# Kernel tuning notes

Hardware: AMD Instinct MI355X
Metric: run time of the kernel (lower is better)

Reference implementation:

```python
import jax, jax.numpy as jnp
import numpy as np
import math

B, T, D, H = 2, 2048, 1024, 16
HD = D // H  # head_dim = 64
DFF = 4 * D
EPS = 1e-5


def gelu_tanh(x):
    c = math.sqrt(2.0 / math.pi)
    return 0.5 * x * (1.0 + jnp.tanh(c * (x + 0.044715 * x ** 3)))


def layernorm(x, scale, shift):
    mean = jnp.mean(x, axis=-1, keepdims=True)
    var = jnp.mean((x - mean) ** 2, axis=-1, keepdims=True)
    return scale * (x - mean) / jnp.sqrt(var + EPS) + shift


def setup_inputs() -> dict:
    key = jax.random.key(0)
    ks = jax.random.split(key, 10)
    s_in = 1.0 / math.sqrt(D)
    s_ff = 1.0 / math.sqrt(DFF)
    return {
        "x": jax.random.normal(ks[0], (B, T, D), dtype=jnp.float32),
        "Wq": jax.random.normal(ks[1], (D, D), dtype=jnp.float32) * s_in,
        "Wk": jax.random.normal(ks[2], (D, D), dtype=jnp.float32) * s_in,
        "Wv": jax.random.normal(ks[3], (D, D), dtype=jnp.float32) * s_in,
        "Wo": jax.random.normal(ks[4], (D, D), dtype=jnp.float32) * s_in,
        "bo": jnp.zeros((D,), dtype=jnp.float32),
        "W1": jax.random.normal(ks[5], (D, DFF), dtype=jnp.float32) * s_in,
        "b1": jnp.zeros((DFF,), dtype=jnp.float32),
        "W2": jax.random.normal(ks[6], (DFF, D), dtype=jnp.float32) * s_ff,
        "b2": jnp.zeros((D,), dtype=jnp.float32),
        "g1": jnp.ones((D,), dtype=jnp.float32),
        "s1": jnp.zeros((D,), dtype=jnp.float32),
        "g2": jnp.ones((D,), dtype=jnp.float32),
        "s2": jnp.zeros((D,), dtype=jnp.float32),
    }


def reference(x, Wq, Wk, Wv, Wo, bo, W1, b1, W2, b2, g1, s1, g2, s2):
    # --- attention sublayer (pre-LN) ---
    h = layernorm(x, g1, s1)
    q = (h @ Wq).reshape(B, T, H, HD).transpose(0, 2, 1, 3)  # [B,H,T,hd]
    k = (h @ Wk).reshape(B, T, H, HD).transpose(0, 2, 1, 3)
    v = (h @ Wv).reshape(B, T, H, HD).transpose(0, 2, 1, 3)
    scores = jnp.einsum('bhqd,bhkd->bhqk', q, k) / math.sqrt(HD)
    causal = jnp.triu(jnp.ones((T, T), dtype=bool), k=1)
    scores = jnp.where(causal, -jnp.inf, scores)
    attn = jax.nn.softmax(scores, axis=-1)
    ctx = jnp.einsum('bhqk,bhkd->bhqd', attn, v)
    ctx = ctx.transpose(0, 2, 1, 3).reshape(B, T, D)
    x = x + (ctx @ Wo + bo)
    # --- feed-forward sublayer (pre-LN) ---
    h2 = layernorm(x, g2, s2)
    ff = gelu_tanh(h2 @ W1 + b1) @ W2 + b2
    return x + ff
```

## Files before the change

### kernel.cpp

```cpp
#include <hip/hip_runtime.h>
#include <cstdint>
#include <cstddef>

typedef unsigned short u16;
typedef __attribute__((ext_vector_type(8))) __bf16 bf16x8;
typedef __attribute__((ext_vector_type(8))) unsigned short u16x8;
typedef __attribute__((ext_vector_type(4))) float f32x4;
typedef __attribute__((ext_vector_type(16))) float f32x16;
typedef __attribute__((ext_vector_type(4))) unsigned short u16x4;
typedef __attribute__((ext_vector_type(2))) int i32x2;

#define DEV __device__ __forceinline__

DEV u16 f2bf(float f) {
  union { float f; unsigned u; } v; v.f = f;
  unsigned r = v.u + 0x7fffu + ((v.u >> 16) & 1u);
  return (u16)(r >> 16);
}

DEV float bf2f(u16 b) {
  unsigned u = ((unsigned)b) << 16;
  union { unsigned u; float f; } v; v.u = u;
  return v.f;
}

DEV void gload_lds16(const void* g, void* l) {
  __builtin_amdgcn_global_load_lds(
      (const __attribute__((address_space(1))) void*)g,
      (__attribute__((address_space(3))) void*)l, 16, 0, 0);
}

DEV float gelu_f(float x) {
  float u = 0.7978845608028654f * (x + 0.044715f * x * x * x);
  float t = exp2f(-2.8853900817779268f * u);
  return x * __builtin_amdgcn_rcpf(1.0f + t);
}

DEV unsigned cvtpk_bf16(float lo, float hi) {
  unsigned u;
  asm("v_cvt_pk_bf16_f32 %0, %1, %2" : "=v"(u) : "v"(lo), "v"(hi));
  return u;
}

__global__ __launch_bounds__(256) void wtrans(const float* __restrict__ W,
                                              u16* __restrict__ Wt, int K, int N) {
  __shared__ float tile[32][33];
  const int n0 = blockIdx.x * 32, k0 = blockIdx.y * 32;
  const int t = threadIdx.x, c = t & 31, r0 = t >> 5;
#pragma unroll
  for (int i = 0; i < 4; ++i) {
    int r = r0 + i * 8;
    tile[r][c] = W[(size_t)(k0 + r) * N + n0 + c];
  }
  __syncthreads();
#pragma unroll
  for (int i = 0; i < 4; ++i) {
    int r = r0 + i * 8;
    Wt[(size_t)(n0 + r) * K + k0 + c] = f2bf(tile[c][r]);
  }
}

__global__ __launch_bounds__(256) void wtrans3(const float* __restrict__ WA,
                                               const float* __restrict__ WB,
                                               const float* __restrict__ WC,
                                               u16* __restrict__ Wt) {
  __shared__ float tile[32][33];
  const int z = blockIdx.z;
  const float* W = (z == 0) ? WA : (z == 1) ? WB : WC;
  u16* out = Wt + (size_t)z * 1024 * 1024;
  const int n0 = blockIdx.x * 32, k0 = blockIdx.y * 32;
  const int t = threadIdx.x, c = t & 31, r0 = t >> 5;
#pragma unroll
  for (int i = 0; i < 4; ++i) {
    int r = r0 + i * 8;
    tile[r][c] = W[(size_t)(k0 + r) * 1024 + n0 + c];
  }
  __syncthreads();
#pragma unroll
  for (int i = 0; i < 4; ++i) {
    int r = r0 + i * 8;
    out[(size_t)(n0 + r) * 1024 + k0 + c] = f2bf(tile[c][r]);
  }
}

__global__ __launch_bounds__(256) void ln_bf16(const float* __restrict__ x,
                                               const float* __restrict__ g,
                                               const float* __restrict__ s,
                                               u16* __restrict__ out) {
  const int row = blockIdx.x, t = threadIdx.x;
  const int l = t & 63, w = t >> 6;
  f32x4 v = *(const f32x4*)(x + (size_t)row * 1024 + t * 4);
  float sm = v.x + v.y + v.z + v.w;
  float s2 = v.x * v.x + v.y * v.y + v.z * v.z + v.w * v.w;
#pragma unroll
  for (int d = 1; d < 64; d <<= 1) { sm += __shfl_xor(sm, d); s2 += __shfl_xor(s2, d); }
  __shared__ float red[8];
  if (l == 0) { red[w] = sm; red[4 + w] = s2; }
  __syncthreads();
  sm = red[0] + red[1] + red[2] + red[3];
  s2 = red[4] + red[5] + red[6] + red[7];
  const float mean = sm * (1.0f / 1024.0f);
  const float rstd = rsqrtf(s2 * (1.0f / 1024.0f) - mean * mean + 1e-5f);
  f32x4 gv = *(const f32x4*)(g + t * 4);
  f32x4 sv = *(const f32x4*)(s + t * 4);
  u16x4 o;
  o.x = f2bf((v.x - mean) * rstd * gv.x + sv.x);
  o.y = f2bf((v.y - mean) * rstd * gv.y + sv.y);
  o.z = f2bf((v.z - mean) * rstd * gv.z + sv.z);
  o.w = f2bf((v.w - mean) * rstd * gv.w + sv.w);
  *(u16x4*)(out + (size_t)row * 1024 + t * 4) = o;
}

template <int EPI>
__global__ __launch_bounds__(256) void gemm_bt(const u16* __restrict__ A,
                                               const u16* __restrict__ Bt,
                                               const float* __restrict__ bias,
                                               const float* __restrict__ resid,
                                               void* __restrict__ outp,
                                               void* __restrict__ outpB,
                                               void* __restrict__ outpC,
                                               void* __restrict__ outpD,
                                               int M, int N, int K) {
  __shared__ alignas(16) u16 As[2][128 * 32];
  __shared__ alignas(16) u16 Bs[2][128 * 32];
  const int tid = threadIdx.x, l = tid & 63, w = tid >> 6;
  const int bm0 = blockIdx.x * 128, bn0 = blockIdx.y * 128;
  const int wm = (w >> 1) * 64, wn = (w & 1) * 64;
  const int lr = l & 15, lk8 = (l >> 4) * 8;

  const int z = blockIdx.z;
  const int Kc = K / gridDim.z;
  const int kbeg = z * Kc, kend = kbeg + Kc;
  void* po = outp;
  if (EPI == 3) po = (z == 0) ? outp : (z == 1) ? outpB : (z == 2) ? outpC : outpD;

  auto STAGE = [&](int buf, int k0) {
#pragma unroll
    for (int c = 0; c < 2; ++c) {
      const int lin = c * 256 + tid;
      const int row = lin >> 2, col = (lin & 3) * 8;
      gload_lds16(A + (size_t)(bm0 + row) * K + k0 + col, (char*)As[buf] + lin * 16);
      gload_lds16(Bt + (size_t)(bn0 + row) * K + k0 + col, (char*)Bs[buf] + lin * 16);
    }
  };

  f32x4 acc[4][4];
#pragma unroll
  for (int i = 0; i < 4; ++i)
#pragma unroll
    for (int j = 0; j < 4; ++j) acc[i][j] = (f32x4){0.f, 0.f, 0.f, 0.f};

  STAGE(0, kbeg);
  if (kbeg + 32 < kend) {
    STAGE(1, kbeg + 32);
    asm volatile("s_waitcnt vmcnt(4)" ::: "memory");
  } else {
    asm volatile("s_waitcnt vmcnt(0)" ::: "memory");
  }
  __builtin_amdgcn_s_barrier();
  __builtin_amdgcn_sched_barrier(0);

  int cur = 0;
  for (int k0 = kbeg; k0 < kend; k0 += 32) {
    bf16x8 af[4], bfv[4];
#pragma unroll
    for (int i = 0; i < 4; ++i) af[i] = *(const bf16x8*)(As[cur] + (wm + i * 16 + lr) * 32 + lk8);
#pragma unroll
    for (int j = 0; j < 4; ++j) bfv[j] = *(const bf16x8*)(Bs[cur] + (wn + j * 16 + lr) * 32 + lk8);
#pragma unroll
    for (int i = 0; i < 4; ++i)
#pragma unroll
      for (int j = 0; j < 4; ++j)
        acc[i][j] = __builtin_amdgcn_mfma_f32_16x16x32_bf16(af[i], bfv[j], acc[i][j], 0, 0, 0);

    if (k0 + 32 < kend) {
      __builtin_amdgcn_sched_barrier(0);
      __builtin_amdgcn_s_barrier();
      if (k0 + 64 < kend) {
        STAGE(cur, k0 + 64);
        asm volatile("s_waitcnt vmcnt(4)" ::: "memory");
      } else {
        asm volatile("s_waitcnt vmcnt(0)" ::: "memory");
      }
      __builtin_amdgcn_s_barrier();
      __builtin_amdgcn_sched_barrier(0);
      cur ^= 1;
    }
  }

#pragma unroll
  for (int i = 0; i < 4; ++i) {
#pragma unroll
    for (int r = 0; r < 4; ++r) {
      const int m = bm0 + wm + i * 16 + (l >> 4) * 4 + r;
#pragma unroll
      for (int j = 0; j < 4; ++j) {
        const int n = bn0 + wn + j * 16 + lr;
        const float va = acc[i][j][r];
        if (EPI == 0) {
          ((u16*)po)[(size_t)m * N + n] = f2bf(va);
        } else if (EPI == 1) {
          ((u16*)po)[(size_t)m * N + n] = f2bf(gelu_f(va + bias[n]));
        } else if (EPI == 2) {
          ((float*)po)[(size_t)m * N + n] = va + bias[n] + resid[(size_t)m * N + n];
        } else {
          ((u16*)po)[(size_t)m * N + n] = f2bf(va);
        }
      }
    }
  }
}

__global__ __launch_bounds__(256) void reduce4(const u16* __restrict__ p0,
                                               const u16* __restrict__ p1,
                                               const u16* __restrict__ p2,
                                               const u16* __restrict__ p3,
                                               const float* __restrict__ bias,
                                               const float* __restrict__ resid,
                                               float* __restrict__ out) {
  const int m = blockIdx.x, t = threadIdx.x;
  const size_t off = (size_t)m * 1024 + t * 4;
  const u16x4 a0 = *(const u16x4*)(p0 + off);
  const u16x4 a1 = *(const u16x4*)(p1 + off);
  const u16x4 a2 = *(const u16x4*)(p2 + off);
  const u16x4 a3 = *(const u16x4*)(p3 + off);
  const f32x4 rv = *(const f32x4*)(resid + off);
  const f32x4 bv = *(const f32x4*)(bias + t * 4);
  f32x4 o;
  o.x = bf2f(a0.x) + bf2f(a1.x) + bf2f(a2.x) + bf2f(a3.x) + bv.x + rv.x;
  o.y = bf2f(a0.y) + bf2f(a1.y) + bf2f(a2.y) + bf2f(a3.y) + bv.y + rv.y;
  o.z = bf2f(a0.z) + bf2f(a1.z) + bf2f(a2.z) + bf2f(a3.z) + bv.z + rv.z;
  o.w = bf2f(a0.w) + bf2f(a1.w) + bf2f(a2.w) + bf2f(a3.w) + bv.w + rv.w;
  *(f32x4*)(out + off) = o;
}

__global__ __launch_bounds__(256) void reduce4_ln(const u16* __restrict__ p0,
                                                  const u16* __restrict__ p1,
                                                  const u16* __restrict__ p2,
                                                  const u16* __restrict__ p3,
                                                  const float* __restrict__ bias,
                                                  const float* __restrict__ resid,
                                                  float* __restrict__ xo,
                                                  const float* __restrict__ g,
                                                  const float* __restrict__ s,
                                                  u16* __restrict__ ho) {
  const int row = blockIdx.x, t = threadIdx.x;
  const int l = t & 63, w = t >> 6;
  const size_t off = (size_t)row * 1024 + t * 4;
  const u16x4 a0 = *(const u16x4*)(p0 + off);
  const u16x4 a1 = *(const u16x4*)(p1 + off);
  const u16x4 a2 = *(const u16x4*)(p2 + off);
  const u16x4 a3 = *(const u16x4*)(p3 + off);
  const f32x4 rv = *(const f32x4*)(resid + off);
  const f32x4 bv = *(const f32x4*)(bias + t * 4);
  f32x4 v;
  v.x = bf2f(a0.x) + bf2f(a1.x) + bf2f(a2.x) + bf2f(a3.x) + bv.x + rv.x;
  v.y = bf2f(a0.y) + bf2f(a1.y) + bf2f(a2.y) + bf2f(a3.y) + bv.y + rv.y;
  v.z = bf2f(a0.z) + bf2f(a1.z) + bf2f(a2.z) + bf2f(a3.z) + bv.z + rv.z;
  v.w = bf2f(a0.w) + bf2f(a1.w) + bf2f(a2.w) + bf2f(a3.w) + bv.w + rv.w;
  *(f32x4*)(xo + off) = v;

  float sm = v.x + v.y + v.z + v.w;
  float s2 = v.x * v.x + v.y * v.y + v.z * v.z + v.w * v.w;
#pragma unroll
  for (int d = 1; d < 64; d <<= 1) { sm += __shfl_xor(sm, d); s2 += __shfl_xor(s2, d); }
  __shared__ float red[8];
  if (l == 0) { red[w] = sm; red[4 + w] = s2; }
  __syncthreads();
  sm = red[0] + red[1] + red[2] + red[3];
  s2 = red[4] + red[5] + red[6] + red[7];
  const float mean = sm * (1.0f / 1024.0f);
  const float rstd = rsqrtf(s2 * (1.0f / 1024.0f) - mean * mean + 1e-5f);
  f32x4 gv = *(const f32x4*)(g + t * 4);
  f32x4 sv = *(const f32x4*)(s + t * 4);
  u16x4 o;
  o.x = f2bf((v.x - mean) * rstd * gv.x + sv.x);
  o.y = f2bf((v.y - mean) * rstd * gv.y + sv.y);
  o.z = f2bf((v.z - mean) * rstd * gv.z + sv.z);
  o.w = f2bf((v.w - mean) * rstd * gv.w + sv.w);
  *(u16x4*)(ho + off) = o;
}

__global__ __launch_bounds__(256) void kvrepack(const u16* __restrict__ qkv,
                                                u16* __restrict__ Kf,
                                                u16* __restrict__ Vf) {
  const int t = blockIdx.x;
  const int bh = blockIdx.y, b = bh >> 4, h = bh & 15;
  const int tid = threadIdx.x;
  u16* kout = Kf + (size_t)bh * 131072;
  u16* vout = Vf + (size_t)bh * 131072;

#pragma unroll
  for (int i = 0; i < 2; ++i) {
    const int s = tid + i * 256;
    const int h2 = s >> 8, kc = (s >> 6) & 3, li = s & 63;
    const int lni = li & 31, hii = li >> 5;
    const u16x8 r = *(const u16x8*)(qkv +
        (size_t)(b * 2048 + t * 64 + h2 * 32 + lni) * 3072 + 1024 + h * 64 + kc * 16 + hii * 8);
    *(u16x8*)(kout + ((size_t)t * 8 + h2 * 4 + kc) * 512 + li * 8) = r;
  }

  __shared__ u16 Vt[64][72];
  {
    const int tok = tid >> 2, dc = (tid & 3) * 16;
    const u16* src = qkv + (size_t)(b * 2048 + t * 64 + tok) * 3072 + 2048 + h * 64 + dc;
    *(u16x8*)&Vt[tok][dc] = *(const u16x8*)src;
    *(u16x8*)&Vt[tok][dc + 8] = *(const u16x8*)(src + 8);
  }
  __syncthreads();
#pragma unroll
  for (int i = 0; i < 2; ++i) {
    const int s = tid + i * 256;
    const int dh = s >> 8, ks = (s >> 6) & 3, li = s & 63;
    const int lni = li & 31, hii = li >> 5;
    u16x8 o;
#pragma unroll
    for (int e = 0; e < 8; ++e) o[e] = Vt[ks * 16 + hii * 8 + e][dh * 32 + lni];
    *(u16x8*)(vout + ((size_t)t * 8 + dh * 4 + ks) * 512 + li * 8) = o;
  }
}

template <int BASE>
DEV bf16x8 pack_pfrag(const f32x16& p, int hi) {
  unsigned C = cvtpk_bf16(p[BASE + 0], p[BASE + 1]);
  unsigned D = cvtpk_bf16(p[BASE + 2], p[BASE + 3]);
  unsigned A = cvtpk_bf16(p[BASE + 4], p[BASE + 5]);
  unsigned B = cvtpk_bf16(p[BASE + 6], p[BASE + 7]);
  unsigned u0, u1, u2, u3;
#if __has_builtin(__builtin_amdgcn_permlane32_swap)
  i32x2 r02 = __builtin_amdgcn_permlane32_swap((int)C, (int)A, false, false);
  i32x2 r13 = __builtin_amdgcn_permlane32_swap((int)D, (int)B, false, false);
  u0 = (unsigned)r02.x; u2 = (unsigned)r02.y;
  u1 = (unsigned)r13.x; u3 = (unsigned)r13.y;
#else
  unsigned pC = (unsigned)__shfl_xor((int)C, 32);
  unsigned pD = (unsigned)__shfl_xor((int)D, 32);
  unsigned pA = (unsigned)__shfl_xor((int)A, 32);
  unsigned pB = (unsigned)__shfl_xor((int)B, 32);
  u0 = hi ? pA : C;  u1 = hi ? pB : D;
  u2 = hi ? A : pC;  u3 = hi ? B : pD;
#endif
  union { unsigned u[4]; bf16x8 v; } res;
  res.u[0] = u0; res.u[1] = u1; res.u[2] = u2; res.u[3] = u3;
  return res.v;
}

__global__ __launch_bounds__(64, 1) void attn_split(const u16* __restrict__ q,
                                                    const u16* __restrict__ kf,
                                                    const u16* __restrict__ vf,
                                                    u16* __restrict__ opart,
                                                    float* __restrict__ mlpart, int ldq) {
  const int xb = blockIdx.x;
  const int qw = 63 - (xb >> 1);
  const int split = xb & 1;
  const int bh = blockIdx.y, b = bh >> 4, h = bh & 15;
  const int l = (int)threadIdx.x & 63;
  const int ln = l & 31, hi = l >> 5;
  const int q0w = qw * 32;
  const int qg = q0w + ln;

  const float qscale = 0.125f * 1.44269504f;
  bf16x8 qf[4];
#pragma unroll
  for (int kc = 0; kc < 4; ++kc) {
    u16x8 raw = *(const u16x8*)(q + (size_t)(b * 2048 + qg) * ldq + h * 64 + kc * 16 + hi * 8);
    union { u16 us[8]; bf16x8 v; } sc;
#pragma unroll
    for (int e = 0; e < 8; ++e) sc.us[e] = f2bf(bf2f(raw[e]) * qscale);
    qf[kc] = sc.v;
  }

  const int nt = (qw >> 1) + 1;
  const int nt0 = nt >> 1;
  const int tb = split ? nt0 : 0;
  const int te = split ? nt : nt0;
  const int dlast = nt - 1;
  const u16* kfp = kf + (size_t)bh * 131072 + l * 8;
  const u16* vfp = vf + (size_t)bh * 131072 + l * 8;

  f32x16 o0, o1;
#pragma unroll
  for (int r = 0; r < 16; ++r) { o0[r] = 0.f; o1[r] = 0.f; }
  float m = -1e30f, lsum = 0.f;

  if (tb < te) {
    bf16x8 ka[4], kb[4];
    {
      const u16* kp = kfp + (size_t)tb * 4096;
#pragma unroll
      for (int kc = 0; kc < 4; ++kc) {
        ka[kc] = *(const bf16x8*)(kp + kc * 512);
        kb[kc] = *(const bf16x8*)(kp + 2048 + kc * 512);
      }
    }

    for (int t = tb; t < te; ++t) {
      const int kv0 = t * 64;
      const bool diag = (t == dlast);
      const bool s1live = !(diag && !(qw & 1));

      const u16* vb = vfp + (size_t)t * 4096;
      bf16x8 v0[4], v1[4];
#pragma unroll
      for (int ks = 0; ks < 4; ++ks) {
        v0[ks] = *(const bf16x8*)(vb + ks * 512);
        v1[ks] = *(const bf16x8*)(vb + 2048 + ks * 512);
      }

      f32x16 s0, s1;
#pragma unroll
      for (int r = 0; r < 16; ++r) { s0[r] = 0.f; s1[r] = 0.f; }
      __builtin_amdgcn_s_setprio(1);
#pragma unroll
      for (int kc = 0; kc < 4; ++kc)
        s0 = __builtin_amdgcn_mfma_f32_32x32x16_bf16(ka[kc], qf[kc], s0, 0, 0, 0);
      if (s1live) {
#pragma unroll
        for (int kc = 0; kc < 4; ++kc)
          s1 = __builtin_amdgcn_mfma_f32_32x32x16_bf16(kb[kc], qf[kc], s1, 0, 0, 0);
      }
      __builtin_amdgcn_s_setprio(0);

      {
        const u16* kn = kfp + (size_t)((t + 1 < te) ? t + 1 : t) * 4096;
#pragma unroll
        for (int kc = 0; kc < 4; ++kc) {
          ka[kc] = *(const bf16x8*)(kn + kc * 512);
          kb[kc] = *(const bf16x8*)(kn + 2048 + kc * 512);
        }
      }

      if (diag) {
#pragma unroll
        for (int r = 0; r < 16; ++r) {
          const int crow = (r & 3) + 8 * (r >> 2) + 4 * hi;
          if (qw & 1) {
            s1[r] = (kv0 + 32 + crow <= qg) ? s1[r] : -1e30f;
          } else {
            s0[r] = (kv0 + crow <= qg) ? s0[r] : -1e30f;
            s1[r] = -1e30f;
          }
        }
      }

      float pm = -1e30f;
#pragma unroll
      for (int r = 0; r < 16; ++r) pm = fmaxf(pm, fmaxf(s0[r], s1[r]));
      pm = fmaxf(pm, __shfl_xor(pm, 32));

      const float mnew = fmaxf(m, pm);
      if (!__all(pm <= m + 8.0f)) {
        const float alpha = exp2f(m - mnew);
        m = mnew;
        lsum *= alpha;
#pragma unroll
        for (int r = 0; r < 16; ++r) { o0[r] *= alpha; o1[r] *= alpha; }
      }

      float ps = 0.f;
#pragma unroll
      for (int r = 0; r < 16; ++r) {
        const float p0 = exp2f(s0[r] - m);
        const float p1 = exp2f(s1[r] - m);
        s0[r] = p0; s1[r] = p1;
        ps += p0 + p1;
      }
      ps += __shfl_xor(ps, 32);
      lsum += ps;

      bf16x8 apv[4];
      apv[0] = pack_pfrag<0>(s0, hi);
      apv[1] = pack_pfrag<8>(s0, hi);
      apv[2] = pack_pfrag<0>(s1, hi);
      apv[3] = pack_pfrag<8>(s1, hi);
      __builtin_amdgcn_s_setprio(1);
#pragma unroll
      for (int ks = 0; ks < 4; ++ks) {
        o0 = __builtin_amdgcn_mfma_f32_32x32x16_bf16(apv[ks], v0[ks], o0, 0, 0, 0);
        o1 = __builtin_amdgcn_mfma_f32_32x32x16_bf16(apv[ks], v1[ks], o1, 0, 0, 0);
      }
      __builtin_amdgcn_s_setprio(0);
    }
  }

  u16* ob = opart + ((size_t)xb * 32 + bh) * 2048;
  float* mlb = mlpart + ((size_t)xb * 32 + bh) * 64;
#pragma unroll
  for (int r = 0; r < 16; ++r) {
    const int crow = (r & 3) + 8 * (r >> 2) + 4 * hi;
    ob[crow * 64 + ln] = f2bf(o0[r]);
    ob[crow * 64 + 32 + ln] = f2bf(o1[r]);
  }
  if (hi == 0) mlb[ln] = m; else mlb[32 + ln] = lsum;
}

__global__ __launch_bounds__(256) void attn_merge(const u16* __restrict__ opart,
                                                  const float* __restrict__ mlpart,
                                                  u16* __restrict__ ctx) {
  const int qw = blockIdx.x, bh = blockIdx.y, b = bh >> 4, h = bh & 15;
  const int tid = threadIdx.x;
  const int q = tid >> 3, dg = (tid & 7) * 8;
  const size_t base0 = (size_t)((63 - qw) * 2) * 32 + bh;
  const size_t base1 = base0 + 32;
  const float m0 = mlpart[base0 * 64 + q], l0 = mlpart[base0 * 64 + 32 + q];
  const float m1 = mlpart[base1 * 64 + q], l1 = mlpart[base1 * 64 + 32 + q];
  const float mn = fmaxf(m0, m1);
  const float f0 = exp2f(m0 - mn), f1 = exp2f(m1 - mn);
  const float linv = 1.0f / (f0 * l0 + f1 * l1);
  const u16x8 a = *(const u16x8*)(opart + base0 * 2048 + q * 64 + dg);
  const u16x8 c = *(const u16x8*)(opart + base1 * 2048 + q * 64 + dg);
  u16x8 o;
#pragma unroll
  for (int e = 0; e < 8; ++e)
    o[e] = f2bf((f0 * bf2f(a[e]) + f1 * bf2f(c[e])) * linv);
  *(u16x8*)(ctx + (size_t)(b * 2048 + qw * 32 + q) * 1024 + h * 64 + dg) = o;
}

extern "C" void kernel_launch(void* const* d_in, const int* in_sizes, int n_in,
                              void* d_out, int out_size, void* d_ws, size_t ws_size,
                              hipStream_t stream) {
  const float* x  = (const float*)d_in[0];
  const float* Wq = (const float*)d_in[1];
  const float* Wk = (const float*)d_in[2];
  const float* Wv = (const float*)d_in[3];
  const float* Wo = (const float*)d_in[4];
  const float* bo = (const float*)d_in[5];
  const float* W1 = (const float*)d_in[6];
  const float* b1 = (const float*)d_in[7];
  const float* W2 = (const float*)d_in[8];
  const float* b2 = (const float*)d_in[9];
  const float* g1 = (const float*)d_in[10];
  const float* s1 = (const float*)d_in[11];
  const float* g2 = (const float*)d_in[12];
  const float* s2 = (const float*)d_in[13];

  char* ws = (char*)d_ws;
  const size_t MB = 1ull << 20;
  u16*  h1    = (u16*)(ws + 0);
  u16*  wqkvT = (u16*)(ws + 8 * MB);
  u16*  woT   = (u16*)(ws + 14 * MB);
  u16*  w1T   = (u16*)(ws + 16 * MB);
  u16*  w2T   = (u16*)(ws + 24 * MB);
  u16*  qkv   = (u16*)(ws + 32 * MB);
  u16*  vfr   = (u16*)(ws + 56 * MB);
  u16*  ctx   = (u16*)(ws + 64 * MB);
  float* x2   = (float*)(ws + 72 * MB);
  u16*  ff1   = (u16*)(ws + 32 * MB);
  u16*  kfr   = h1;
  u16*   opart  = (u16*)(ws + 72 * MB);
  float* mlpart = (float*)(ws + 8 * MB);
  u16*  op0   = (u16*)(ws + 0);
  u16*  op1   = (u16*)(ws + 32 * MB);
  u16*  op2   = (u16*)(ws + 40 * MB);
  u16*  op3   = (u16*)(ws + 56 * MB);
  u16*  wp0   = (u16*)(ws + 0);
  u16*  wp1   = (u16*)(ws + 8 * MB);
  u16*  wp2   = (u16*)(ws + 16 * MB);
  u16*  wp3   = (u16*)(ws + 64 * MB);

  const dim3 blk(256);

  wtrans3<<<dim3(32, 32, 3), blk, 0, stream>>>(Wq, Wk, Wv, wqkvT);
  wtrans<<<dim3(32, 32),  blk, 0, stream>>>(Wo, woT, 1024, 1024);
  wtrans<<<dim3(128, 32), blk, 0, stream>>>(W1, w1T, 1024, 4096);
  wtrans<<<dim3(32, 128), blk, 0, stream>>>(W2, w2T, 4096, 1024);

  ln_bf16<<<dim3(4096), blk, 0, stream>>>(x, g1, s1, h1);

  gemm_bt<0><<<dim3(32, 24), blk, 0, stream>>>(h1, wqkvT, nullptr, nullptr,
                                               (void*)qkv, nullptr, nullptr, nullptr,
                                               4096, 3072, 1024);

  kvrepack<<<dim3(32, 32), blk, 0, stream>>>(qkv, kfr, vfr);

  attn_split<<<dim3(128, 32), dim3(64), 0, stream>>>(qkv, kfr, vfr, opart, mlpart, 3072);
  attn_merge<<<dim3(64, 32), blk, 0, stream>>>(opart, mlpart, ctx);

  gemm_bt<3><<<dim3(32, 8, 4), blk, 0, stream>>>(ctx, woT, nullptr, nullptr,
                                                 (void*)op0, (void*)op1, (void*)op2, (void*)op3,
                                                 4096, 1024, 1024);

  reduce4_ln<<<dim3(4096), blk, 0, stream>>>(op0, op1, op2, op3, bo, x, x2, g2, s2, h1);

  gemm_bt<1><<<dim3(32, 32), blk, 0, stream>>>(h1, w1T, b1, nullptr,
                                               (void*)ff1, nullptr, nullptr, nullptr,
                                               4096, 4096, 1024);

  gemm_bt<3><<<dim3(32, 8, 4), blk, 0, stream>>>(ff1, w2T, nullptr, nullptr,
                                                 (void*)wp0, (void*)wp1, (void*)wp2, (void*)wp3,
                                                 4096, 1024, 4096);

  reduce4<<<dim3(4096), blk, 0, stream>>>(wp0, wp1, wp2, wp3, b2, x2, (float*)d_out);
}
```

Before: 285.4 us.

## Triple-buffer GEMM LDS staging with XOR swizzle and relax attention launch bounds

```diff
diff --git a/kernel.cpp b/kernel.cpp
--- a/kernel.cpp
+++ b/kernel.cpp
@@ -121,26 +121,29 @@
                                                void* __restrict__ outpC,
                                                void* __restrict__ outpD,
                                                int M, int N, int K) {
-  __shared__ alignas(16) u16 As[2][128 * 32];
-  __shared__ alignas(16) u16 Bs[2][128 * 32];
+  __shared__ alignas(16) u16 As[3][128 * 32];
+  __shared__ alignas(16) u16 Bs[3][128 * 32];
   const int tid = threadIdx.x, l = tid & 63, w = tid >> 6;
   const int bm0 = blockIdx.x * 128, bn0 = blockIdx.y * 128;
   const int wm = (w >> 1) * 64, wn = (w & 1) * 64;
-  const int lr = l & 15, lk8 = (l >> 4) * 8;
+  const int lr = l & 15;
+  const int sg = (((l >> 4) ^ (l & 3))) * 8;
 
   const int z = blockIdx.z;
   const int Kc = K / gridDim.z;
-  const int kbeg = z * Kc, kend = kbeg + Kc;
+  const int kbeg = z * Kc;
+  const int nt = Kc >> 5;
   void* po = outp;
   if (EPI == 3) po = (z == 0) ? outp : (z == 1) ? outpB : (z == 2) ? outpC : outpD;
 
-  auto STAGE = [&](int buf, int k0) {
+  auto STAGE = [&](int slot, int k0) {
 #pragma unroll
     for (int c = 0; c < 2; ++c) {
       const int lin = c * 256 + tid;
-      const int row = lin >> 2, col = (lin & 3) * 8;
-      gload_lds16(A + (size_t)(bm0 + row) * K + k0 + col, (char*)As[buf] + lin * 16);
-      gload_lds16(Bt + (size_t)(bn0 + row) * K + k0 + col, (char*)Bs[buf] + lin * 16);
+      const int row = lin >> 2, s = lin & 3;
+      const int gs = s ^ (row & 3);
+      gload_lds16(A + (size_t)(bm0 + row) * K + k0 + gs * 8, (char*)As[slot] + lin * 16);
+      gload_lds16(Bt + (size_t)(bn0 + row) * K + k0 + gs * 8, (char*)Bs[slot] + lin * 16);
     }
   };
 
@@ -151,7 +154,7 @@
     for (int j = 0; j < 4; ++j) acc[i][j] = (f32x4){0.f, 0.f, 0.f, 0.f};
 
   STAGE(0, kbeg);
-  if (kbeg + 32 < kend) {
+  if (nt > 1) {
     STAGE(1, kbeg + 32);
     asm volatile("s_waitcnt vmcnt(4)" ::: "memory");
   } else {
@@ -160,31 +163,31 @@
   __builtin_amdgcn_s_barrier();
   __builtin_amdgcn_sched_barrier(0);
 
-  int cur = 0;
-  for (int k0 = kbeg; k0 < kend; k0 += 32) {
+  for (int t = 0; t < nt; ++t) {
+    const int cur = t % 3;
+    if (t + 2 < nt) STAGE((t + 2) % 3, kbeg + (t + 2) * 32);
+
     bf16x8 af[4], bfv[4];
 #pragma unroll
-    for (int i = 0; i < 4; ++i) af[i] = *(const bf16x8*)(As[cur] + (wm + i * 16 + lr) * 32 + lk8);
-#pragma unroll
-    for (int j = 0; j < 4; ++j) bfv[j] = *(const bf16x8*)(Bs[cur] + (wn + j * 16 + lr) * 32 + lk8);
+    for (int i = 0; i < 4; ++i) af[i] = *(const bf16x8*)(As[cur] + (wm + i * 16 + lr) * 32 + sg);
+#pragma unroll
+    for (int j = 0; j < 4; ++j) bfv[j] = *(const bf16x8*)(Bs[cur] + (wn + j * 16 + lr) * 32 + sg);
 #pragma unroll
     for (int i = 0; i < 4; ++i)
 #pragma unroll
       for (int j = 0; j < 4; ++j)
         acc[i][j] = __builtin_amdgcn_mfma_f32_16x16x32_bf16(af[i], bfv[j], acc[i][j], 0, 0, 0);
 
-    if (k0 + 32 < kend) {
-      __builtin_amdgcn_sched_barrier(0);
-      __builtin_amdgcn_s_barrier();
-      if (k0 + 64 < kend) {
-        STAGE(cur, k0 + 64);
+    __builtin_amdgcn_sched_barrier(0);
+    __builtin_amdgcn_s_barrier();
+    if (t + 1 < nt) {
+      if (t + 2 < nt) {
         asm volatile("s_waitcnt vmcnt(4)" ::: "memory");
       } else {
         asm volatile("s_waitcnt vmcnt(0)" ::: "memory");
       }
       __builtin_amdgcn_s_barrier();
       __builtin_amdgcn_sched_barrier(0);
-      cur ^= 1;
     }
   }
 
@@ -345,7 +348,7 @@
   return res.v;
 }
 
-__global__ __launch_bounds__(64, 1) void attn_split(const u16* __restrict__ q,
+__global__ __launch_bounds__(64, 2) void attn_split(const u16* __restrict__ q,
                                                     const u16* __restrict__ kf,
                                                     const u16* __restrict__ vf,
                                                     u16* __restrict__ opart,
```

Result: no change. 289.1 us (+1.3%).
